# Kernel tuning notes

Hardware: AMD Instinct MI355X
Metric: run time of the kernel (lower is better)

## Reference

```python
import jax, jax.numpy as jnp
import numpy as np

B, N, D, H = 16, 256, 128, 8
HD = D // H
PAIR_DIMS = [64, 64, 64]
EPS = 1e-8


def _pairwise_lv_fts(x):
    # x: [B, 4, N] four-vectors (px, py, pz, E); returns [B, N, N, 4] = (lnkt, lnz, lndelta, lnm2)
    px, py, pz, e = x[:, 0], x[:, 1], x[:, 2], x[:, 3]
    pt = jnp.sqrt(jnp.clip(px ** 2 + py ** 2, EPS))          # [B, N]
    rap = 0.5 * jnp.log1p(2.0 * pz / jnp.clip(e - pz, 1e-20))
    phi = jnp.arctan2(py, px)
    d_rap = rap[:, :, None] - rap[:, None, :]                 # [B, N, N]
    d_phi = (phi[:, :, None] - phi[:, None, :] + np.pi) % (2.0 * np.pi) - np.pi
    delta = jnp.sqrt(d_rap ** 2 + d_phi ** 2)
    lndelta = jnp.log(jnp.clip(delta, EPS))
    ptmin = jnp.minimum(pt[:, :, None], pt[:, None, :])
    lnkt = jnp.log(jnp.clip(ptmin * delta, EPS))
    lnz = jnp.log(jnp.clip(ptmin / jnp.clip(pt[:, :, None] + pt[:, None, :], EPS), EPS))
    es = e[:, :, None] + e[:, None, :]
    pxs = px[:, :, None] + px[:, None, :]
    pys = py[:, :, None] + py[:, None, :]
    pzs = pz[:, :, None] + pz[:, None, :]
    lnm2 = jnp.log(jnp.clip(es ** 2 - pxs ** 2 - pys ** 2 - pzs ** 2, EPS))
    return jnp.stack([lnkt, lnz, lndelta, lnm2], axis=-1)


def setup_inputs() -> dict:
    key = jax.random.key(0)
    ks = jax.random.split(key, 12)
    p3 = jax.random.normal(ks[0], (B, 3, N), jnp.float32)
    e = jnp.sqrt((p3 ** 2).sum(1, keepdims=True)
                 + jnp.abs(jax.random.normal(ks[1], (B, 1, N), jnp.float32)) ** 2 + 0.1)
    x_pf = jnp.concatenate([p3, e], axis=1)                   # physical four-vectors [B,4,N]
    x_feat = jax.random.normal(ks[2], (B, N, D), jnp.float32) * 0.02
    dims = [4] + PAIR_DIMS + [H]
    pw = {}
    for i in range(4):
        pw[f"pair_w{i}"] = jax.random.normal(ks[3 + i], (dims[i], dims[i + 1]), jnp.float32) / np.sqrt(dims[i])
        pw[f"pair_b{i}"] = jnp.zeros((dims[i + 1],), jnp.float32)
    proj = {n: jax.random.normal(k, (D, D), jnp.float32) / np.sqrt(D)
            for n, k in zip(["wq", "wk", "wv", "wo"], jax.random.split(ks[7], 4))}
    bias = {n: jnp.zeros((D,), jnp.float32) for n in ["bq", "bk", "bv", "bo"]}
    return dict(x_pf=x_pf, x_feat=x_feat, **pw, **proj, **bias)


def reference(x_pf, x_feat, pair_w0, pair_b0, pair_w1, pair_b1, pair_w2, pair_b2,
              pair_w3, pair_b3, wq, wk, wv, wo, bq, bk, bv, bo):
    # pairwise Lorentz-invariant features -> dense attention bias
    u = _pairwise_lv_fts(x_pf)                                # [B, N, N, 4]
    for w, b in ((pair_w0, pair_b0), (pair_w1, pair_b1), (pair_w2, pair_b2)):
        u = jax.nn.gelu(u @ w + b)
    attn_bias = jnp.transpose(u @ pair_w3 + pair_b3, (0, 3, 1, 2))  # [B, H, N, N]
    # multi-head attention with pairwise bias
    q = (x_feat @ wq + bq).reshape(B, N, H, HD)
    k = (x_feat @ wk + bk).reshape(B, N, H, HD)
    v = (x_feat @ wv + bv).reshape(B, N, H, HD)
    scores = jnp.einsum("bihd,bjhd->bhij", q, k) / np.sqrt(HD) + attn_bias
    attn = jax.nn.softmax(scores, axis=-1)
    out = jnp.einsum("bhij,bjhd->bihd", attn, v).reshape(B, N, D)
    return out @ wo + bo                                      # [B, N, D]
```

## Files before the change

kernel.cpp:

```cpp
#include <hip/hip_runtime.h>
#include <hip/hip_bf16.h>
#include <math.h>

#define B_ 16
#define N_ 256
#define D_ 128
#define H_ 8
#define HD_ 16
#define EPS_ 1e-8f
#define PI_F 3.14159265358979323846f
#define TWO_PI_F 6.28318530717958647692f
#define INV_TWO_PI_F 0.15915494309189533577f
#define L2E_F 1.4426950408889634f

#define OFF_PT   0
#define OFF_RAP  4096
#define OFF_PHI  8192
#define OFF_PX   12288
#define OFF_PY   16384
#define OFF_PZ   20480
#define OFF_E    24576
#define OFF_Q    28672
#define OFF_K    (28672 + 524288)
#define OFF_V    (28672 + 2*524288)
#define OFF_BIAS (28672 + 3*524288)
#define OFF_AO   (OFF_BIAS + 8388608)
#define OFF_WPACK (OFF_AO + 524288)

#define UA0  0
#define UA1H 2048
#define UA1L 6144
#define UA2H 10240
#define UA2L 14336
#define UA3H 18432
#define UA3L 19456
#define UQKV 20480

typedef _Float16 f16x8 __attribute__((ext_vector_type(8)));
typedef _Float16 f16x4 __attribute__((ext_vector_type(4)));
typedef _Float16 f16x2 __attribute__((ext_vector_type(2)));
typedef __attribute__((ext_vector_type(4))) float f4;
typedef __attribute__((ext_vector_type(4))) unsigned int u4;

__device__ __forceinline__ unsigned pkh2(float a, float b) {
    f16x2 v = { (_Float16)a, (_Float16)b };
    return __builtin_bit_cast(unsigned, v);
}
__device__ __forceinline__ float f16res(float x) {
    return x - (float)(_Float16)x;
}

__device__ __forceinline__ float gelu_f(float x) {
    float y2 = x * fmaf(0.10294337f, x * x, 2.3022079f);
    float e = __builtin_amdgcn_exp2f(-y2);
    return x * __builtin_amdgcn_rcpf(1.0f + e);
}


__global__ __launch_bounds__(256) void k_prep(
    const float* __restrict__ w0, const float* __restrict__ w1,
    const float* __restrict__ w2, const float* __restrict__ w3,
    const float* __restrict__ wq, const float* __restrict__ wk,
    const float* __restrict__ wv, const float* __restrict__ wo,
    const float* __restrict__ x_pf,
    _Float16* __restrict__ wp, float* __restrict__ ws) {
    if (blockIdx.x >= 64) {
        int idx = (blockIdx.x - 64) * 256 + threadIdx.x;
        int b = idx >> 8, n = idx & 255;
        const float* base = x_pf + (size_t)b * 4 * N_;
        float px = base[0 * N_ + n];
        float py = base[1 * N_ + n];
        float pz = base[2 * N_ + n];
        float e  = base[3 * N_ + n];
        float pt  = sqrtf(fmaxf(px * px + py * py, EPS_));
        float rap = 0.5f * log1pf(2.0f * pz / fmaxf(e - pz, 1e-20f));
        float phi = atan2f(py, px);
        ws[OFF_PT  + idx] = pt;
        ws[OFF_RAP + idx] = rap;
        ws[OFF_PHI + idx] = phi;
        ws[OFF_PX  + idx] = px;
        ws[OFF_PY  + idx] = py;
        ws[OFF_PZ  + idx] = pz;
        ws[OFF_E   + idx] = e;
        return;
    }
    int id0 = blockIdx.x * 256 + threadIdx.x;
    const int gs = 64 * 256;
    for (int e = id0; e < 2048; e += gs) {
        int fi = e >> 3, j = e & 7;
        int mt = fi >> 6, lane = fi & 63;
        int q = lane >> 4, ln = lane & 15;
        int m = mt * 16 + ln;
        _Float16 v = (_Float16)0.0f;
        if (q == 0) v = (j < 4) ? (_Float16)w0[j * 64 + m]
                                : (_Float16)f16res(w0[(j - 4) * 64 + m]);
        else if (q == 1) v = (j < 4) ? (_Float16)w0[j * 64 + m] : (_Float16)0.0f;
        wp[UA0 + e] = v;
    }
    for (int e = id0; e < 4096; e += gs) {
        int fi = e >> 3, j = e & 7;
        int mt = fi >> 7, ks = (fi >> 6) & 1, lane = fi & 63;
        int q = lane >> 4;
        int m = mt * 16 + (lane & 15);
        int k = (2 * (j >> 2) + ks) * 16 + q * 4 + (j & 3);
        float x1 = w1[k * 64 + m];
        wp[UA1H + e] = (_Float16)x1;
        wp[UA1L + e] = (_Float16)f16res(x1);
        float x2 = w2[k * 64 + m];
        wp[UA2H + e] = (_Float16)x2;
        wp[UA2L + e] = (_Float16)f16res(x2);
    }
    for (int e = id0; e < 1024; e += gs) {
        int fi = e >> 3, j = e & 7;
        int ks = fi >> 6, lane = fi & 63;
        int q = lane >> 4;
        int m = lane & 15;
        int k = (2 * (j >> 2) + ks) * 16 + q * 4 + (j & 3);
        float x = (m < 8) ? w3[k * 8 + m] : 0.0f;
        wp[UA3H + e] = (_Float16)x;
        wp[UA3L + e] = (_Float16)f16res(x);
    }
    const float* mats[4] = { wq, wk, wv, wo };
#pragma unroll 1
    for (int mi = 0; mi < 4; ++mi) {
        const float* W = mats[mi];
        _Float16* dst = wp + UQKV + mi * 32768;
        for (int e = id0; e < 16384; e += gs) {
            int fi = e >> 3, j = e & 7;
            int mt = fi >> 8, ks = (fi >> 6) & 3, lane = fi & 63;
            int k = ks * 32 + ((lane >> 4) << 3) + j;
            int o = mt * 16 + (lane & 15);
            float x = W[k * 128 + o];
            dst[e] = (_Float16)x;
            dst[16384 + e] = (_Float16)f16res(x);
        }
    }
}

__device__ __forceinline__ void epi_frag(const f4 (&acc)[4][4], const float* __restrict__ bg,
                                         int q, u4 (&Bu)[4][2]) {
#pragma unroll
    for (int mt = 0; mt < 4; ++mt) {
        f4 bv = *(const f4*)&bg[mt * 16 + q * 4];
        int ks = mt & 1, hi = (mt >> 1) * 2;
#pragma unroll
        for (int nt = 0; nt < 4; ++nt) {
            float g0 = gelu_f(acc[mt][nt][0] + bv[0]);
            float g1 = gelu_f(acc[mt][nt][1] + bv[1]);
            float g2 = gelu_f(acc[mt][nt][2] + bv[2]);
            float g3 = gelu_f(acc[mt][nt][3] + bv[3]);
            Bu[nt][ks][hi]     = pkh2(g0, g1);
            Bu[nt][ks][hi + 1] = pkh2(g2, g3);
        }
    }
}

__device__ __forceinline__ void mid_layer(f4 (&acc)[4][4],
                                          const _Float16* __restrict__ wh,
                                          const _Float16* __restrict__ wl,
                                          int lane, const u4 (&Bu)[4][2]) {
    const f4 zero4 = { 0.f, 0.f, 0.f, 0.f };
#pragma unroll
    for (int mt = 0; mt < 4; ++mt) {
        f16x8 ah0 = *(const f16x8*)&wh[((mt * 2 + 0) * 64 + lane) * 8];
        f16x8 ah1 = *(const f16x8*)&wh[((mt * 2 + 1) * 64 + lane) * 8];
        f16x8 al0 = *(const f16x8*)&wl[((mt * 2 + 0) * 64 + lane) * 8];
        f16x8 al1 = *(const f16x8*)&wl[((mt * 2 + 1) * 64 + lane) * 8];
#pragma unroll
        for (int nt = 0; nt < 4; ++nt) {
            f16x8 b0 = __builtin_bit_cast(f16x8, Bu[nt][0]);
            f16x8 b1 = __builtin_bit_cast(f16x8, Bu[nt][1]);
            f4 c = zero4;
            c = __builtin_amdgcn_mfma_f32_16x16x32_f16(ah0, b0, c, 0, 0, 0);
            c = __builtin_amdgcn_mfma_f32_16x16x32_f16(al0, b0, c, 0, 0, 0);
            c = __builtin_amdgcn_mfma_f32_16x16x32_f16(ah1, b1, c, 0, 0, 0);
            c = __builtin_amdgcn_mfma_f32_16x16x32_f16(al1, b1, c, 0, 0, 0);
            acc[mt][nt] = c;
        }
    }
}

__device__ __forceinline__ void mfma_gemm64x16(
    const float* __restrict__ xrow, const _Float16* __restrict__ wpm,
    int mtbase, const float* __restrict__ biasv, float* __restrict__ outp, int lane) {
    int q = lane >> 4;
    const f4 zero4 = { 0.f, 0.f, 0.f, 0.f };
    f16x8 Bh[4], Bl[4];
#pragma unroll
    for (int ks = 0; ks < 4; ++ks) {
        const float* p = xrow + ks * 32 + q * 8;
        float4 xa = ((const float4*)p)[0];
        float4 xb = ((const float4*)p)[1];
        u4 hu = { pkh2(xa.x, xa.y), pkh2(xa.z, xa.w), pkh2(xb.x, xb.y), pkh2(xb.z, xb.w) };
        u4 lu = { pkh2(f16res(xa.x), f16res(xa.y)), pkh2(f16res(xa.z), f16res(xa.w)),
                  pkh2(f16res(xb.x), f16res(xb.y)), pkh2(f16res(xb.z), f16res(xb.w)) };
        Bh[ks] = __builtin_bit_cast(f16x8, hu);
        Bl[ks] = __builtin_bit_cast(f16x8, lu);
    }
#pragma unroll
    for (int mtl = 0; mtl < 4; ++mtl) {
        int mt = mtbase + mtl;
        f4 c = zero4;
#pragma unroll
        for (int ks = 0; ks < 4; ++ks) {
            const _Float16* fa = wpm + ((size_t)((mt * 4 + ks) * 64 + lane)) * 8;
            f16x8 ah = *(const f16x8*)fa;
            f16x8 al = *(const f16x8*)(fa + 16384);
            c = __builtin_amdgcn_mfma_f32_16x16x32_f16(ah, Bh[ks], c, 0, 0, 0);
            c = __builtin_amdgcn_mfma_f32_16x16x32_f16(ah, Bl[ks], c, 0, 0, 0);
            c = __builtin_amdgcn_mfma_f32_16x16x32_f16(al, Bh[ks], c, 0, 0, 0);
        }
        f4 bv = *(const f4*)&biasv[mtl * 16 + q * 4];
        f4 r = c + bv;
        *(f4*)(outp + mtl * 16 + q * 4) = r;
    }
}

__global__ __launch_bounds__(256, 4) void k_pair_qkv(
    const float* __restrict__ ws, const _Float16* __restrict__ wp,
    const float* __restrict__ b0g, const float* __restrict__ b1g,
    const float* __restrict__ b2g, const float* __restrict__ b3g,
    float* __restrict__ bias_out,
    const float* __restrict__ xf,
    const float* __restrict__ bqv, const float* __restrict__ bkv, const float* __restrict__ bvv,
    float* __restrict__ qkv_out) {
    int tid = threadIdx.x;
    int lane = tid & 63;
    int ln = lane & 15, q = lane >> 4;

    if (blockIdx.x < 384) {
        int wid = blockIdx.x * 4 + (tid >> 6);
        int og = wid % 6, tg = wid / 6;
        int mi = og >> 1, ch = og & 1;
        const _Float16* wpm = wp + UQKV + mi * 32768;
        const float* bias = (mi == 0) ? bqv : ((mi == 1) ? bkv : bvv);
        float* outb = qkv_out + OFF_Q + (size_t)mi * 524288;
        size_t tok = (size_t)(tg * 16 + ln);
        mfma_gemm64x16(xf + tok * 128, wpm, ch * 4, bias + ch * 64,
                       outb + tok * 128 + ch * 64, lane);
        return;
    }

    int w2 = (blockIdx.x - 384) * 4 + (tid >> 6);
    int b = w2 / 640;
    int w = w2 - b * 640;
    int it, rr, nj;
    if (w < 256)      { it = 0; rr = w;       nj = 4; }
    else if (w < 448) { it = 1; rr = w - 256; nj = 3; }
    else if (w < 576) { it = 2; rr = w - 448; nj = 2; }
    else              { it = 3; rr = w - 576; nj = 1; }
    int i  = it * 64 + rr / nj;
    int jt = it + rr % nj;
    int j0 = jt * 64;
    int row = (b << 8) + i;

    unsigned FH01, FH23, FL01, FL23;
    {
        int ib = row;
        int jb = (b << 8) + j0 + lane;
        float pt_i = ws[OFF_PT + ib],  rap_i = ws[OFF_RAP + ib], phi_i = ws[OFF_PHI + ib];
        float px_i = ws[OFF_PX + ib],  py_i  = ws[OFF_PY  + ib];
        float pz_i = ws[OFF_PZ + ib],  e_i   = ws[OFF_E   + ib];
        float pt_j = ws[OFF_PT + jb],  rap_j = ws[OFF_RAP + jb], phi_j = ws[OFF_PHI + jb];
        float px_j = ws[OFF_PX + jb],  py_j  = ws[OFF_PY  + jb];
        float pz_j = ws[OFF_PZ + jb],  e_j   = ws[OFF_E   + jb];

        float drap = rap_i - rap_j;
        float xw = phi_i - phi_j + PI_F;
        float mw = xw - TWO_PI_F * floorf(xw * INV_TWO_PI_F);
        float dphi = mw - PI_F;
        float delta = sqrtf(drap * drap + dphi * dphi);
        float f2 = __logf(fmaxf(delta, EPS_));
        float ptmin = fminf(pt_i, pt_j);
        float f0 = __logf(fmaxf(ptmin * delta, EPS_));
        float f1 = __logf(fmaxf(ptmin / fmaxf(pt_i + pt_j, EPS_), EPS_));
        float es = e_i + e_j, pxs = px_i + px_j, pys = py_i + py_j, pzs = pz_i + pz_j;
        float f3 = __logf(fmaxf(es * es - pxs * pxs - pys * pys - pzs * pzs, EPS_));

        FH01 = pkh2(f0, f1);
        FH23 = pkh2(f2, f3);
        FL01 = pkh2(f16res(f0), f16res(f1));
        FL23 = pkh2(f16res(f2), f16res(f3));
    }

    f4 acc[4][4];
    const f4 zero4 = { 0.f, 0.f, 0.f, 0.f };

    {
        f16x8 a0[4];
#pragma unroll
        for (int mt = 0; mt < 4; ++mt)
            a0[mt] = *(const f16x8*)&wp[UA0 + (mt * 64 + lane) * 8];
#pragma unroll
        for (int nt = 0; nt < 4; ++nt) {
            int src = nt * 16 + ln;
            unsigned h01 = (unsigned)__shfl((int)FH01, src);
            unsigned h23 = (unsigned)__shfl((int)FH23, src);
            unsigned l01 = (unsigned)__shfl((int)FL01, src);
            unsigned l23 = (unsigned)__shfl((int)FL23, src);
            u4 bu;
            bu[0] = (q == 0) ? h01 : ((q == 1) ? l01 : 0u);
            bu[1] = (q == 0) ? h23 : ((q == 1) ? l23 : 0u);
            bu[2] = (q == 0) ? h01 : 0u;
            bu[3] = (q == 0) ? h23 : 0u;
            f16x8 bf = __builtin_bit_cast(f16x8, bu);
#pragma unroll
            for (int mt = 0; mt < 4; ++mt)
                acc[mt][nt] = __builtin_amdgcn_mfma_f32_16x16x32_f16(a0[mt], bf, zero4, 0, 0, 0);
        }
    }

    u4 Bu[4][2];
    epi_frag(acc, b0g, q, Bu);
    mid_layer(acc, wp + UA1H, wp + UA1L, lane, Bu);
    epi_frag(acc, b1g, q, Bu);
    mid_layer(acc, wp + UA2H, wp + UA2L, lane, Bu);
    epi_frag(acc, b2g, q, Bu);

    {
        f16x8 a3h0 = *(const f16x8*)&wp[UA3H + (0 * 64 + lane) * 8];
        f16x8 a3h1 = *(const f16x8*)&wp[UA3H + (1 * 64 + lane) * 8];
        f16x8 a3l0 = *(const f16x8*)&wp[UA3L + (0 * 64 + lane) * 8];
        f16x8 a3l1 = *(const f16x8*)&wp[UA3L + (1 * 64 + lane) * 8];
        f4 acc3[4];
#pragma unroll
        for (int nt = 0; nt < 4; ++nt) {
            f16x8 b0 = __builtin_bit_cast(f16x8, Bu[nt][0]);
            f16x8 b1 = __builtin_bit_cast(f16x8, Bu[nt][1]);
            f4 c = zero4;
            c = __builtin_amdgcn_mfma_f32_16x16x32_f16(a3h0, b0, c, 0, 0, 0);
            c = __builtin_amdgcn_mfma_f32_16x16x32_f16(a3l0, b0, c, 0, 0, 0);
            c = __builtin_amdgcn_mfma_f32_16x16x32_f16(a3h1, b1, c, 0, 0, 0);
            c = __builtin_amdgcn_mfma_f32_16x16x32_f16(a3l1, b1, c, 0, 0, 0);
            acc3[nt] = c;
        }
        if (q < 2) {
            f4 b3v = *(const f4*)&b3g[q * 4];
            bool mirror = (jt != it);
#pragma unroll
            for (int nt = 0; nt < 4; ++nt) {
                int jc = j0 + nt * 16 + ln;
#pragma unroll
                for (int r = 0; r < 4; ++r) {
                    int out = q * 4 + r;
                    float val = acc3[nt][r] + b3v[r];
                    size_t basebh = ((size_t)(b * H_ + out)) * N_;
                    bias_out[(basebh + i) * N_ + jc] = val;
                    if (mirror) bias_out[(basebh + jc) * N_ + i] = val;
                }
            }
        }
    }
}

#define SVT 264
__global__ __launch_bounds__(256) void k_attn(const float* __restrict__ ws,
                                              float* __restrict__ wso) {
    __shared__ __align__(16) _Float16 Vt[16 * SVT];
    int tid = threadIdx.x;
    int blk = blockIdx.x;
    int ib = blk & 3;
    int bh = blk >> 2;
    int b = bh >> 3, h = bh & 7;

    {
        const float* vr = ws + OFF_V + ((size_t)(b * 256 + tid)) * 128 + h * 16;
        float4 v0 = ((const float4*)vr)[0];
        float4 v1 = ((const float4*)vr)[1];
        float4 v2 = ((const float4*)vr)[2];
        float4 v3 = ((const float4*)vr)[3];
        Vt[ 0 * SVT + tid] = (_Float16)v0.x;  Vt[ 1 * SVT + tid] = (_Float16)v0.y;
        Vt[ 2 * SVT + tid] = (_Float16)v0.z;  Vt[ 3 * SVT + tid] = (_Float16)v0.w;
        Vt[ 4 * SVT + tid] = (_Float16)v1.x;  Vt[ 5 * SVT + tid] = (_Float16)v1.y;
        Vt[ 6 * SVT + tid] = (_Float16)v1.z;  Vt[ 7 * SVT + tid] = (_Float16)v1.w;
        Vt[ 8 * SVT + tid] = (_Float16)v2.x;  Vt[ 9 * SVT + tid] = (_Float16)v2.y;
        Vt[10 * SVT + tid] = (_Float16)v2.z;  Vt[11 * SVT + tid] = (_Float16)v2.w;
        Vt[12 * SVT + tid] = (_Float16)v3.x;  Vt[13 * SVT + tid] = (_Float16)v3.y;
        Vt[14 * SVT + tid] = (_Float16)v3.z;  Vt[15 * SVT + tid] = (_Float16)v3.w;
    }
    __syncthreads();

    int lane = tid & 63, w = tid >> 6;
    int ln = lane & 15, q = lane >> 4;
    int i0 = ib * 64 + w * 16;
    const f4 zero4 = { 0.f, 0.f, 0.f, 0.f };

    f16x8 Bq;
    {
        const float* qr = ws + OFF_Q + ((size_t)(b * 256 + i0 + ln)) * 128 + h * 16 + (q & 1) * 8;
        float4 qa = ((const float4*)qr)[0];
        float4 qb = ((const float4*)qr)[1];
        u4 hu = { pkh2(qa.x, qa.y), pkh2(qa.z, qa.w), pkh2(qb.x, qb.y), pkh2(qb.z, qb.w) };
        Bq = __builtin_bit_cast(f16x8, hu);
    }

    f4 accs[16];
    const float* Kbase = ws + OFF_K + ((size_t)(b * 256)) * 128 + h * 16;
    const float* bb = ws + OFF_BIAS + ((size_t)(bh * 256 + i0 + ln)) * 256 + q * 4;
#pragma unroll
    for (int mt = 0; mt < 16; ++mt) {
        const float* kr = Kbase + (size_t)(mt * 16 + ln) * 128 + (q & 1) * 8;
        float4 ka = ((const float4*)kr)[0];
        float4 kb = ((const float4*)kr)[1];
        u4 hu = { pkh2(ka.x, ka.y), pkh2(ka.z, ka.w), pkh2(kb.x, kb.y), pkh2(kb.z, kb.w) };
        u4 lu = { pkh2(f16res(ka.x), f16res(ka.y)), pkh2(f16res(ka.z), f16res(ka.w)),
                  pkh2(f16res(kb.x), f16res(kb.y)), pkh2(f16res(kb.z), f16res(kb.w)) };
        u4 au;
        bool qlo = (q < 2);
        au[0] = qlo ? hu[0] : lu[0];
        au[1] = qlo ? hu[1] : lu[1];
        au[2] = qlo ? hu[2] : lu[2];
        au[3] = qlo ? hu[3] : lu[3];
        f16x8 Ak = __builtin_bit_cast(f16x8, au);
        f4 s = __builtin_amdgcn_mfma_f32_16x16x32_f16(Ak, Bq, zero4, 0, 0, 0);
        f4 bias4 = *(const f4*)&bb[mt * 16];
#pragma unroll
        for (int r = 0; r < 4; ++r) s[r] = fmaf(s[r], 0.25f, bias4[r]);
        accs[mt] = s;
    }

    float mx = accs[0][0];
#pragma unroll
    for (int mt = 0; mt < 16; ++mt)
#pragma unroll
        for (int r = 0; r < 4; ++r) mx = fmaxf(mx, accs[mt][r]);
    mx = fmaxf(mx, __shfl_xor(mx, 16));
    mx = fmaxf(mx, __shfl_xor(mx, 32));
    float nms = -mx * L2E_F;
    float l = 0.0f;
#pragma unroll
    for (int mt = 0; mt < 16; ++mt) {
#pragma unroll
        for (int r = 0; r < 4; ++r) {
            float p = __builtin_amdgcn_exp2f(fmaf(accs[mt][r], L2E_F, nms));
            accs[mt][r] = p;
            l += p;
        }
    }
    l += __shfl_xor(l, 16);
    l += __shfl_xor(l, 32);
    float inv = __builtin_amdgcn_rcpf(l);

    f4 o = zero4;
#pragma unroll
    for (int ks = 0; ks < 8; ++ks) {
        u4 bp = { pkh2(accs[2 * ks][0], accs[2 * ks][1]),
                  pkh2(accs[2 * ks][2], accs[2 * ks][3]),
                  pkh2(accs[2 * ks + 1][0], accs[2 * ks + 1][1]),
                  pkh2(accs[2 * ks + 1][2], accs[2 * ks + 1][3]) };
        int vb = ln * SVT + 32 * ks + 4 * q;
        f16x4 lo4 = *(const f16x4*)&Vt[vb];
        f16x4 hi4 = *(const f16x4*)&Vt[vb + 16];
        f16x8 av;
        av[0] = lo4[0]; av[1] = lo4[1]; av[2] = lo4[2]; av[3] = lo4[3];
        av[4] = hi4[0]; av[5] = hi4[1]; av[6] = hi4[2]; av[7] = hi4[3];
        o = __builtin_amdgcn_mfma_f32_16x16x32_f16(av, __builtin_bit_cast(f16x8, bp), o, 0, 0, 0);
    }
    f4 res = o * inv;
    *(f4*)(wso + OFF_AO + ((size_t)(b * 256 + i0 + ln)) * 128 + h * 16 + q * 4) = res;
}

__global__ __launch_bounds__(256) void k_out(
    const float* __restrict__ ws, const _Float16* __restrict__ wp,
    const float* __restrict__ bo, float* __restrict__ out) {
    int tid = threadIdx.x;
    int lane = tid & 63, ln = lane & 15;
    int wid = blockIdx.x * 4 + (tid >> 6);
    int og = wid & 1, tg = wid >> 1;
    const _Float16* wpm = wp + UQKV + 3 * 32768;
    size_t tok = (size_t)(tg * 16 + ln);
    mfma_gemm64x16(ws + OFF_AO + tok * 128, wpm, og * 4, bo + og * 64,
                   out + tok * 128 + og * 64, lane);
}

extern "C" void kernel_launch(void* const* d_in, const int* in_sizes, int n_in,
                              void* d_out, int out_size, void* d_ws, size_t ws_size,
                              hipStream_t stream) {
    const float* x_pf   = (const float*)d_in[0];
    const float* x_feat = (const float*)d_in[1];
    const float* w0 = (const float*)d_in[2];
    const float* b0 = (const float*)d_in[3];
    const float* w1 = (const float*)d_in[4];
    const float* b1 = (const float*)d_in[5];
    const float* w2 = (const float*)d_in[6];
    const float* b2 = (const float*)d_in[7];
    const float* w3 = (const float*)d_in[8];
    const float* b3 = (const float*)d_in[9];
    const float* wq = (const float*)d_in[10];
    const float* wk = (const float*)d_in[11];
    const float* wv = (const float*)d_in[12];
    const float* wo = (const float*)d_in[13];
    const float* bq = (const float*)d_in[14];
    const float* bk = (const float*)d_in[15];
    const float* bv = (const float*)d_in[16];
    const float* bo = (const float*)d_in[17];
    float* ws  = (float*)d_ws;
    float* out = (float*)d_out;
    _Float16* wpack = (_Float16*)(ws + OFF_WPACK);

    hipLaunchKernelGGL(k_prep, dim3(80), dim3(256), 0, stream,
                       w0, w1, w2, w3, wq, wk, wv, wo, x_pf, wpack, ws);
    hipLaunchKernelGGL(k_pair_qkv, dim3(384 + 2560), dim3(256), 0, stream,
                       ws, wpack, b0, b1, b2, b3, ws + OFF_BIAS,
                       x_feat, bq, bk, bv, ws);
    hipLaunchKernelGGL(k_attn, dim3(512), dim3(256), 0, stream, ws, ws);
    hipLaunchKernelGGL(k_out, dim3(128), dim3(256), 0, stream, ws, wpack, bo, out);
}
```

Before: 174.8 us.

## Store Q/K/V as packed fp16 and drop mirrored bias writes

The QKV projection now writes Q and V as fp16 and K as an fp16 hi/lo split, so attention loads half-width data and skips per-element conversion. The pair-bias kernel no longer writes the transposed mirror of off-diagonal tiles. Instead, attention reads lower-triangle bias blocks with strided transposed loads. This cuts bias store traffic and QKV bandwidth, at the cost of uncoalesced strided reads in the attention kernel.

New measurement: 161.4 us. 1.08x faster.

```diff
diff --git a/kernel.cpp b/kernel.cpp
--- a/kernel.cpp
+++ b/kernel.cpp
@@ -21,8 +21,6 @@
 #define OFF_PZ   20480
 #define OFF_E    24576
 #define OFF_Q    28672
-#define OFF_K    (28672 + 524288)
-#define OFF_V    (28672 + 2*524288)
 #define OFF_BIAS (28672 + 3*524288)
 #define OFF_AO   (OFF_BIAS + 8388608)
 #define OFF_WPACK (OFF_AO + 524288)
@@ -180,9 +178,9 @@
     }
 }
 
-__device__ __forceinline__ void mfma_gemm64x16(
+__device__ __forceinline__ void mfma_core64x16(
     const float* __restrict__ xrow, const _Float16* __restrict__ wpm,
-    int mtbase, const float* __restrict__ biasv, float* __restrict__ outp, int lane) {
+    int mtbase, const float* __restrict__ biasv, int lane, f4 (&cc)[4]) {
     int q = lane >> 4;
     const f4 zero4 = { 0.f, 0.f, 0.f, 0.f };
     f16x8 Bh[4], Bl[4];
@@ -211,8 +209,7 @@
             c = __builtin_amdgcn_mfma_f32_16x16x32_f16(al, Bh[ks], c, 0, 0, 0);
         }
         f4 bv = *(const f4*)&biasv[mtl * 16 + q * 4];
-        f4 r = c + bv;
-        *(f4*)(outp + mtl * 16 + q * 4) = r;
+        cc[mtl] = c + bv;
     }
 }
 
@@ -223,7 +220,8 @@
     float* __restrict__ bias_out,
     const float* __restrict__ xf,
     const float* __restrict__ bqv, const float* __restrict__ bkv, const float* __restrict__ bvv,
-    float* __restrict__ qkv_out) {
+    _Float16* __restrict__ qh, _Float16* __restrict__ kh,
+    _Float16* __restrict__ kl, _Float16* __restrict__ vh) {
     int tid = threadIdx.x;
     int lane = tid & 63;
     int ln = lane & 15, q = lane >> 4;
@@ -234,10 +232,24 @@
         int mi = og >> 1, ch = og & 1;
         const _Float16* wpm = wp + UQKV + mi * 32768;
         const float* bias = (mi == 0) ? bqv : ((mi == 1) ? bkv : bvv);
-        float* outb = qkv_out + OFF_Q + (size_t)mi * 524288;
         size_t tok = (size_t)(tg * 16 + ln);
-        mfma_gemm64x16(xf + tok * 128, wpm, ch * 4, bias + ch * 64,
-                       outb + tok * 128 + ch * 64, lane);
+        f4 cc[4];
+        mfma_core64x16(xf + tok * 128, wpm, ch * 4, bias + ch * 64, lane, cc);
+        _Float16* hout = (mi == 0) ? qh : ((mi == 1) ? kh : vh);
+#pragma unroll
+        for (int mtl = 0; mtl < 4; ++mtl) {
+            size_t off = tok * 128 + ch * 64 + mtl * 16 + q * 4;
+            f16x4 hv;
+#pragma unroll
+            for (int r = 0; r < 4; ++r) hv[r] = (_Float16)cc[mtl][r];
+            *(f16x4*)&hout[off] = hv;
+            if (mi == 1) {
+                f16x4 lv;
+#pragma unroll
+                for (int r = 0; r < 4; ++r) lv[r] = (_Float16)(cc[mtl][r] - (float)hv[r]);
+                *(f16x4*)&kl[off] = lv;
+            }
+        }
         return;
     }
 
@@ -336,17 +348,13 @@
         }
         if (q < 2) {
             f4 b3v = *(const f4*)&b3g[q * 4];
-            bool mirror = (jt != it);
 #pragma unroll
             for (int nt = 0; nt < 4; ++nt) {
                 int jc = j0 + nt * 16 + ln;
 #pragma unroll
                 for (int r = 0; r < 4; ++r) {
                     int out = q * 4 + r;
-                    float val = acc3[nt][r] + b3v[r];
-                    size_t basebh = ((size_t)(b * H_ + out)) * N_;
-                    bias_out[(basebh + i) * N_ + jc] = val;
-                    if (mirror) bias_out[(basebh + jc) * N_ + i] = val;
+                    bias_out[(((size_t)(b * H_ + out)) * N_ + i) * N_ + jc] = acc3[nt][r] + b3v[r];
                 }
             }
         }
@@ -354,8 +362,11 @@
 }
 
 #define SVT 264
-__global__ __launch_bounds__(256) void k_attn(const float* __restrict__ ws,
-                                              float* __restrict__ wso) {
+__global__ __launch_bounds__(256) void k_attn(
+    const float* __restrict__ ws,
+    const _Float16* __restrict__ qh, const _Float16* __restrict__ kh,
+    const _Float16* __restrict__ kl, const _Float16* __restrict__ vh,
+    float* __restrict__ wso) {
     __shared__ __align__(16) _Float16 Vt[16 * SVT];
     int tid = threadIdx.x;
     int blk = blockIdx.x;
@@ -364,19 +375,14 @@
     int b = bh >> 3, h = bh & 7;
 
     {
-        const float* vr = ws + OFF_V + ((size_t)(b * 256 + tid)) * 128 + h * 16;
-        float4 v0 = ((const float4*)vr)[0];
-        float4 v1 = ((const float4*)vr)[1];
-        float4 v2 = ((const float4*)vr)[2];
-        float4 v3 = ((const float4*)vr)[3];
-        Vt[ 0 * SVT + tid] = (_Float16)v0.x;  Vt[ 1 * SVT + tid] = (_Float16)v0.y;
-        Vt[ 2 * SVT + tid] = (_Float16)v0.z;  Vt[ 3 * SVT + tid] = (_Float16)v0.w;
-        Vt[ 4 * SVT + tid] = (_Float16)v1.x;  Vt[ 5 * SVT + tid] = (_Float16)v1.y;
-        Vt[ 6 * SVT + tid] = (_Float16)v1.z;  Vt[ 7 * SVT + tid] = (_Float16)v1.w;
-        Vt[ 8 * SVT + tid] = (_Float16)v2.x;  Vt[ 9 * SVT + tid] = (_Float16)v2.y;
-        Vt[10 * SVT + tid] = (_Float16)v2.z;  Vt[11 * SVT + tid] = (_Float16)v2.w;
-        Vt[12 * SVT + tid] = (_Float16)v3.x;  Vt[13 * SVT + tid] = (_Float16)v3.y;
-        Vt[14 * SVT + tid] = (_Float16)v3.z;  Vt[15 * SVT + tid] = (_Float16)v3.w;
+        const _Float16* vr = vh + ((size_t)(b * 256 + tid)) * 128 + h * 16;
+        f16x8 v0 = *(const f16x8*)vr;
+        f16x8 v1 = *(const f16x8*)(vr + 8);
+#pragma unroll
+        for (int d = 0; d < 8; ++d) {
+            Vt[d * SVT + tid] = v0[d];
+            Vt[(8 + d) * SVT + tid] = v1[d];
+        }
     }
     __syncthreads();
 
@@ -387,33 +393,32 @@
 
     f16x8 Bq;
     {
-        const float* qr = ws + OFF_Q + ((size_t)(b * 256 + i0 + ln)) * 128 + h * 16 + (q & 1) * 8;
-        float4 qa = ((const float4*)qr)[0];
-        float4 qb = ((const float4*)qr)[1];
-        u4 hu = { pkh2(qa.x, qa.y), pkh2(qa.z, qa.w), pkh2(qb.x, qb.y), pkh2(qb.z, qb.w) };
-        Bq = __builtin_bit_cast(f16x8, hu);
+        f16x4 qa = *(const f16x4*)&qh[((size_t)(b * 256 + i0 + ln)) * 128 + h * 16 + (q & 1) * 8];
+        f16x4 qb = *(const f16x4*)&qh[((size_t)(b * 256 + i0 + ln)) * 128 + h * 16 + (q & 1) * 8 + 4];
+        f16x8 t;
+        t[0] = qa[0]; t[1] = qa[1]; t[2] = qa[2]; t[3] = qa[3];
+        t[4] = qb[0]; t[5] = qb[1]; t[6] = qb[2]; t[7] = qb[3];
+        Bq = t;
     }
 
     f4 accs[16];
-    const float* Kbase = ws + OFF_K + ((size_t)(b * 256)) * 128 + h * 16;
+    const _Float16* kbase = (q < 2 ? kh : kl) + ((size_t)(b * 256)) * 128 + h * 16 + (q & 1) * 8;
     const float* bb = ws + OFF_BIAS + ((size_t)(bh * 256 + i0 + ln)) * 256 + q * 4;
+    const float* tbb = ws + OFF_BIAS + ((size_t)bh) * 65536 + (i0 + ln);
 #pragma unroll
     for (int mt = 0; mt < 16; ++mt) {
-        const float* kr = Kbase + (size_t)(mt * 16 + ln) * 128 + (q & 1) * 8;
-        float4 ka = ((const float4*)kr)[0];
-        float4 kb = ((const float4*)kr)[1];
-        u4 hu = { pkh2(ka.x, ka.y), pkh2(ka.z, ka.w), pkh2(kb.x, kb.y), pkh2(kb.z, kb.w) };
-        u4 lu = { pkh2(f16res(ka.x), f16res(ka.y)), pkh2(f16res(ka.z), f16res(ka.w)),
-                  pkh2(f16res(kb.x), f16res(kb.y)), pkh2(f16res(kb.z), f16res(kb.w)) };
-        u4 au;
-        bool qlo = (q < 2);
-        au[0] = qlo ? hu[0] : lu[0];
-        au[1] = qlo ? hu[1] : lu[1];
-        au[2] = qlo ? hu[2] : lu[2];
-        au[3] = qlo ? hu[3] : lu[3];
-        f16x8 Ak = __builtin_bit_cast(f16x8, au);
+        f16x8 Ak = *(const f16x8*)&kbase[(size_t)(mt * 16 + ln) * 128];
         f4 s = __builtin_amdgcn_mfma_f32_16x16x32_f16(Ak, Bq, zero4, 0, 0, 0);
-        f4 bias4 = *(const f4*)&bb[mt * 16];
+        f4 bias4;
+        if ((mt >> 2) < ib) {
+            const float* tb = tbb + (size_t)(mt * 16 + q * 4) * 256;
+            bias4[0] = tb[0];
+            bias4[1] = tb[256];
+            bias4[2] = tb[512];
+            bias4[3] = tb[768];
+        } else {
+            bias4 = *(const f4*)&bb[mt * 16];
+        }
 #pragma unroll
         for (int r = 0; r < 4; ++r) s[r] = fmaf(s[r], 0.25f, bias4[r]);
         accs[mt] = s;
@@ -464,13 +469,16 @@
     const float* __restrict__ ws, const _Float16* __restrict__ wp,
     const float* __restrict__ bo, float* __restrict__ out) {
     int tid = threadIdx.x;
-    int lane = tid & 63, ln = lane & 15;
+    int lane = tid & 63, ln = lane & 15, q = lane >> 4;
     int wid = blockIdx.x * 4 + (tid >> 6);
     int og = wid & 1, tg = wid >> 1;
     const _Float16* wpm = wp + UQKV + 3 * 32768;
     size_t tok = (size_t)(tg * 16 + ln);
-    mfma_gemm64x16(ws + OFF_AO + tok * 128, wpm, og * 4, bo + og * 64,
-                   out + tok * 128 + og * 64, lane);
+    f4 cc[4];
+    mfma_core64x16(ws + OFF_AO + tok * 128, wpm, og * 4, bo + og * 64, lane, cc);
+#pragma unroll
+    for (int mtl = 0; mtl < 4; ++mtl)
+        *(f4*)(out + tok * 128 + og * 64 + mtl * 16 + q * 4) = cc[mtl];
 }
 
 extern "C" void kernel_launch(void* const* d_in, const int* in_sizes, int n_in,
@@ -497,12 +505,16 @@
     float* ws  = (float*)d_ws;
     float* out = (float*)d_out;
     _Float16* wpack = (_Float16*)(ws + OFF_WPACK);
+    _Float16* qh = (_Float16*)(ws + OFF_Q);
+    _Float16* kh = qh + 524288;
+    _Float16* kl = kh + 524288;
+    _Float16* vh = kl + 524288;
 
     hipLaunchKernelGGL(k_prep, dim3(80), dim3(256), 0, stream,
                        w0, w1, w2, w3, wq, wk, wv, wo, x_pf, wpack, ws);
     hipLaunchKernelGGL(k_pair_qkv, dim3(384 + 2560), dim3(256), 0, stream,
                        ws, wpack, b0, b1, b2, b3, ws + OFF_BIAS,
-                       x_feat, bq, bk, bv, ws);
-    hipLaunchKernelGGL(k_attn, dim3(512), dim3(256), 0, stream, ws, ws);
+                       x_feat, bq, bk, bv, qh, kh, kl, vh);
+    hipLaunchKernelGGL(k_attn, dim3(512), dim3(256), 0, stream, ws, qh, kh, kl, vh, ws);
     hipLaunchKernelGGL(k_out, dim3(128), dim3(256), 0, stream, ws, wpack, bo, out);
 }
```
